# Kernel optimization log

Hardware: AMD Instinct MI355X
Metric: run time of the kernel (lower is better)

## Reference

```python
import jax, jax.numpy as jnp
import numpy as np

N, E, IN, H, D, ED = 50000, 800000, 128, 4, 16, 16
HD = H * D


def setup_inputs() -> dict:
    key = jax.random.key(0)
    ks = jax.random.split(key, 12)
    s_in = 1.0 / np.sqrt(IN).astype(np.float32)
    s_ed = 1.0 / np.sqrt(ED).astype(np.float32)
    return {
        "x": jax.random.normal(ks[0], (N, IN), jnp.float32),
        "edge_index": jax.random.randint(ks[1], (2, E), 0, N, dtype=jnp.int32),
        "edge_attr": jnp.ones((E, ED), jnp.float32),
        "Wq": jax.random.normal(ks[2], (IN, HD), jnp.float32) * s_in,
        "bq": jnp.zeros((HD,), jnp.float32),
        "Wk": jax.random.normal(ks[3], (IN, HD), jnp.float32) * s_in,
        "bk": jnp.zeros((HD,), jnp.float32),
        "Wv": jax.random.normal(ks[4], (IN, HD), jnp.float32) * s_in,
        "bv": jnp.zeros((HD,), jnp.float32),
        "We": jax.random.normal(ks[5], (ED, HD), jnp.float32) * s_ed,
        "Wskip": jax.random.normal(ks[6], (IN, HD), jnp.float32) * s_in,
        "bskip": jnp.zeros((HD,), jnp.float32),
    }


def reference(x, edge_index, edge_attr, Wq, bq, Wk, bk, Wv, bv, We, Wskip, bskip):
    n = x.shape[0]
    src, dst = edge_index[0], edge_index[1]  # x_j = src, x_i = dst (source_to_target)
    q = (x @ Wq + bq).reshape(n, H, D)
    k = (x @ Wk + bk).reshape(n, H, D)
    v = (x @ Wv + bv).reshape(n, H, D)
    e = (edge_attr @ We).reshape(-1, H, D)  # [E,H,D]

    k_j = k[src] + e                         # [E,H,D]
    v_j = v[src] + e                         # [E,H,D]
    q_i = q[dst]                             # [E,H,D]

    alpha = jnp.sum(q_i * k_j, axis=-1) / jnp.sqrt(jnp.float32(D))  # [E,H]
    # segment softmax over incoming edges per destination node
    amax = jax.ops.segment_max(alpha, dst, num_segments=n)          # [N,H]
    amax = jnp.where(jnp.isfinite(amax), amax, 0.0)
    ex = jnp.exp(alpha - amax[dst])                                 # [E,H]
    denom = jax.ops.segment_sum(ex, dst, num_segments=n)           # [N,H]
    alpha_sm = ex / (denom[dst] + 1e-16)                            # [E,H]

    msg = alpha_sm[..., None] * v_j                                 # [E,H,D]
    out = jax.ops.segment_sum(msg, dst, num_segments=n)            # [N,H,D]
    out = out.reshape(n, HD) + (x @ Wskip + bskip)                  # root/skip connection
    return out, edge_index, alpha_sm
```

## Files before the change

kernel.cpp:

```cpp
#include <hip/hip_runtime.h>


__global__ __launch_bounds__(256) void gemm_qkvs(
    const float* __restrict__ x,
    const float* __restrict__ Wq, const float* __restrict__ bq,
    const float* __restrict__ Wk, const float* __restrict__ bk,
    const float* __restrict__ Wv, const float* __restrict__ bv,
    const float* __restrict__ Wsk, const float* __restrict__ bsk,
    float* __restrict__ q, float* __restrict__ k, float* __restrict__ v,
    float* __restrict__ skip, float* __restrict__ macc,
    float* __restrict__ denom, int N)
{
    __shared__ float Xl[64 * 128];
    const int tid  = threadIdx.x;
    const int base = blockIdx.x * 64;
    const int nvalid = min(64, N - base);

    for (int i = tid; i < 64 * 32; i += 256) {
        int node = i >> 5;
        float4 val = make_float4(0.f, 0.f, 0.f, 0.f);
        if (node < nvalid)
            val = reinterpret_cast<const float4*>(x)[(size_t)(base + node) * 32 + (i & 31)];
        reinterpret_cast<float4*>(Xl)[i] = val;
    }
    __syncthreads();

    const int wave = tid >> 6;
    const int lane = tid & 63;
    const int c   = lane * 4;
    const int arr = c >> 6;
    const int cc  = c & 63;
    const float* W; const float* B; float* O;
    if (arr == 0)      { W = Wq;  B = bq;  O = q; }
    else if (arr == 1) { W = Wk;  B = bk;  O = k; }
    else if (arr == 2) { W = Wv;  B = bv;  O = v; }
    else               { W = Wsk; B = bsk; O = skip; }

    float acc[16][4];
    #pragma unroll
    for (int n = 0; n < 16; n++) {
        acc[n][0] = 0.f; acc[n][1] = 0.f; acc[n][2] = 0.f; acc[n][3] = 0.f;
    }

    const float* Xw = Xl + wave * 16 * 128;

    for (int kk = 0; kk < 128; kk += 4) {
        float4 w0 = *reinterpret_cast<const float4*>(W + (kk + 0) * 64 + cc);
        float4 w1 = *reinterpret_cast<const float4*>(W + (kk + 1) * 64 + cc);
        float4 w2 = *reinterpret_cast<const float4*>(W + (kk + 2) * 64 + cc);
        float4 w3 = *reinterpret_cast<const float4*>(W + (kk + 3) * 64 + cc);
        #pragma unroll
        for (int n = 0; n < 16; n++) {
            float4 xv = *reinterpret_cast<const float4*>(Xw + n * 128 + kk);
            acc[n][0] += xv.x * w0.x + xv.y * w1.x + xv.z * w2.x + xv.w * w3.x;
            acc[n][1] += xv.x * w0.y + xv.y * w1.y + xv.z * w2.y + xv.w * w3.y;
            acc[n][2] += xv.x * w0.z + xv.y * w1.z + xv.z * w2.z + xv.w * w3.z;
            acc[n][3] += xv.x * w0.w + xv.y * w1.w + xv.z * w2.w + xv.w * w3.w;
        }
    }

    const float4 zero4 = make_float4(0.f, 0.f, 0.f, 0.f);
    float4 bias = *reinterpret_cast<const float4*>(B + cc);
    #pragma unroll
    for (int n = 0; n < 16; n++) {
        int node = base + wave * 16 + n;
        if (node < N) {
            float4 r = make_float4(acc[n][0] + bias.x, acc[n][1] + bias.y,
                                   acc[n][2] + bias.z, acc[n][3] + bias.w);
            *reinterpret_cast<float4*>(O + (size_t)node * 64 + cc) = r;
            if (arr == 0)
                *reinterpret_cast<float4*>(macc + (size_t)node * 64 + cc) = zero4;
            if (arr == 1 && cc == 0)
                *reinterpret_cast<float4*>(denom + (size_t)node * 4) = zero4;
        }
    }
}

__global__ __launch_bounds__(256) void edge_fused(
    const int* __restrict__ ei, const float* __restrict__ ea,
    const float* __restrict__ We,
    const float* __restrict__ q, const float* __restrict__ k,
    const float* __restrict__ v,
    float* __restrict__ exa,
    float* __restrict__ denom,
    float* __restrict__ macc,
    int E)
{
    const int tid  = threadIdx.x;
    const int lane = tid & 63;

    float WeR[16];
    #pragma unroll
    for (int j = 0; j < 16; j++) WeR[j] = We[j * 64 + lane];

    const int ed = blockIdx.x * 4 + (tid >> 6);
    if (ed >= E) return;

    const int src = ei[ed];
    const int dst = ei[E + ed];

    const float4* eap = reinterpret_cast<const float4*>(ea + (size_t)ed * 16);
    float4 a0 = eap[0], a1 = eap[1], a2 = eap[2], a3 = eap[3];
    float et = a0.x * WeR[0]  + a0.y * WeR[1]  + a0.z * WeR[2]  + a0.w * WeR[3]
             + a1.x * WeR[4]  + a1.y * WeR[5]  + a1.z * WeR[6]  + a1.w * WeR[7]
             + a2.x * WeR[8]  + a2.y * WeR[9]  + a2.z * WeR[10] + a2.w * WeR[11]
             + a3.x * WeR[12] + a3.y * WeR[13] + a3.z * WeR[14] + a3.w * WeR[15];

    const float kj = k[(size_t)src * 64 + lane] + et;
    const float vj = v[(size_t)src * 64 + lane] + et;
    const float qi = q[(size_t)dst * 64 + lane];

    float p = qi * kj;
    p += __shfl_xor(p, 8);
    p += __shfl_xor(p, 4);
    p += __shfl_xor(p, 2);
    p += __shfl_xor(p, 1);

    const float e1 = __expf(p * 0.25f);

    atomicAdd(&macc[(size_t)dst * 64 + lane], e1 * vj);

    if ((lane & 15) == 0) {
        const int h = lane >> 4;
        exa[(size_t)ed * 4 + h] = e1;
        atomicAdd(&denom[(size_t)dst * 4 + h], e1);
    }
}

__global__ __launch_bounds__(256) void fin_edges(
    const int* __restrict__ ei, const float* __restrict__ denom,
    float* __restrict__ asm_io, float* __restrict__ ei_out, int E)
{
    int e = blockIdx.x * 256 + threadIdx.x;
    if (e >= E) return;
    int s = ei[e];
    int d = ei[E + e];

    float4 a  = *reinterpret_cast<float4*>(asm_io + (size_t)e * 4);
    float4 dn = *reinterpret_cast<const float4*>(denom + (size_t)d * 4);
    a.x /= (dn.x + 1e-16f);
    a.y /= (dn.y + 1e-16f);
    a.z /= (dn.z + 1e-16f);
    a.w /= (dn.w + 1e-16f);
    *reinterpret_cast<float4*>(asm_io + (size_t)e * 4) = a;

    ei_out[e]     = (float)s;
    ei_out[E + e] = (float)d;
}

__global__ __launch_bounds__(256) void fin_out(
    const float* __restrict__ skip, const float* __restrict__ denom,
    float* __restrict__ out_io, int total)
{
    int i = blockIdx.x * 256 + threadIdx.x;
    if (i >= total) return;
    int node = i >> 6, h = (i & 63) >> 4;
    out_io[i] = out_io[i] / (denom[node * 4 + h] + 1e-16f) + skip[i];
}

extern "C" void kernel_launch(void* const* d_in, const int* in_sizes, int n_in,
                              void* d_out, int out_size, void* d_ws, size_t ws_size,
                              hipStream_t stream)
{
    const float* x   = (const float*)d_in[0];
    const int*   ei  = (const int*)  d_in[1];
    const float* ea  = (const float*)d_in[2];
    const float* Wq  = (const float*)d_in[3];
    const float* bq  = (const float*)d_in[4];
    const float* Wk  = (const float*)d_in[5];
    const float* bk  = (const float*)d_in[6];
    const float* Wv  = (const float*)d_in[7];
    const float* bv  = (const float*)d_in[8];
    const float* We  = (const float*)d_in[9];
    const float* Wsk = (const float*)d_in[10];
    const float* bsk = (const float*)d_in[11];

    const int N = in_sizes[0] / 128;
    const int E = in_sizes[1] / 2;

    float* out     = (float*)d_out;
    float* ei_out  = out + (size_t)N * 64;
    float* asm_out = ei_out + (size_t)2 * E;

    float* q     = (float*)d_ws;
    float* k     = q + (size_t)N * 64;
    float* v     = k + (size_t)N * 64;
    float* skip  = v + (size_t)N * 64;
    float* denom = skip + (size_t)N * 64;

    int nb1 = (N + 63) / 64;
    gemm_qkvs<<<nb1, 256, 0, stream>>>(x, Wq, bq, Wk, bk, Wv, bv, Wsk, bsk,
                                       q, k, v, skip, out, denom, N);

    int nb2 = (E + 3) / 4;
    edge_fused<<<nb2, 256, 0, stream>>>(ei, ea, We, q, k, v, asm_out, denom, out, E);

    fin_edges<<<(E + 255) / 256, 256, 0, stream>>>(ei, denom, asm_out, ei_out, E);
    fin_out<<<(N * 64 + 255) / 256, 256, 0, stream>>>(skip, denom, out, N * 64);
}
```

Before: 502.5 us.

## Store q/k/v in fp16 and process two edges per wave

The projection kernel now writes q, k and v as half precision, which halves the bytes moved by the random gathers in the edge kernel. The skip projection stays fp32. The GEMM tile shrinks from 64 to 32 nodes per block, and each wave in the edge kernel now handles two edges, so more independent loads and atomics are in flight. The cost is fp16 rounding error on the attention logits and messages, plus more register use per edge thread.

```diff
diff --git a/kernel.cpp b/kernel.cpp
--- a/kernel.cpp
+++ b/kernel.cpp
@@ -1,5 +1,7 @@
 #include <hip/hip_runtime.h>
 
+
+typedef __attribute__((ext_vector_type(4))) _Float16 half4;
 
 __global__ __launch_bounds__(256) void gemm_qkvs(
     const float* __restrict__ x,
@@ -7,16 +9,17 @@
     const float* __restrict__ Wk, const float* __restrict__ bk,
     const float* __restrict__ Wv, const float* __restrict__ bv,
     const float* __restrict__ Wsk, const float* __restrict__ bsk,
-    float* __restrict__ q, float* __restrict__ k, float* __restrict__ v,
+    _Float16* __restrict__ qh, _Float16* __restrict__ kh,
+    _Float16* __restrict__ vh,
     float* __restrict__ skip, float* __restrict__ macc,
     float* __restrict__ denom, int N)
 {
-    __shared__ float Xl[64 * 128];
+    __shared__ float Xl[32 * 128];
     const int tid  = threadIdx.x;
-    const int base = blockIdx.x * 64;
-    const int nvalid = min(64, N - base);
-
-    for (int i = tid; i < 64 * 32; i += 256) {
+    const int base = blockIdx.x * 32;
+    const int nvalid = min(32, N - base);
+
+    for (int i = tid; i < 32 * 32; i += 256) {
         int node = i >> 5;
         float4 val = make_float4(0.f, 0.f, 0.f, 0.f);
         if (node < nvalid)
@@ -30,19 +33,19 @@
     const int c   = lane * 4;
     const int arr = c >> 6;
     const int cc  = c & 63;
-    const float* W; const float* B; float* O;
-    if (arr == 0)      { W = Wq;  B = bq;  O = q; }
-    else if (arr == 1) { W = Wk;  B = bk;  O = k; }
-    else if (arr == 2) { W = Wv;  B = bv;  O = v; }
-    else               { W = Wsk; B = bsk; O = skip; }
-
-    float acc[16][4];
+    const float* W; const float* B;
+    if (arr == 0)      { W = Wq;  B = bq;  }
+    else if (arr == 1) { W = Wk;  B = bk;  }
+    else if (arr == 2) { W = Wv;  B = bv;  }
+    else               { W = Wsk; B = bsk; }
+
+    float acc[8][4];
     #pragma unroll
-    for (int n = 0; n < 16; n++) {
+    for (int n = 0; n < 8; n++) {
         acc[n][0] = 0.f; acc[n][1] = 0.f; acc[n][2] = 0.f; acc[n][3] = 0.f;
     }
 
-    const float* Xw = Xl + wave * 16 * 128;
+    const float* Xw = Xl + wave * 8 * 128;
 
     for (int kk = 0; kk < 128; kk += 4) {
         float4 w0 = *reinterpret_cast<const float4*>(W + (kk + 0) * 64 + cc);
@@ -50,7 +53,7 @@
         float4 w2 = *reinterpret_cast<const float4*>(W + (kk + 2) * 64 + cc);
         float4 w3 = *reinterpret_cast<const float4*>(W + (kk + 3) * 64 + cc);
         #pragma unroll
-        for (int n = 0; n < 16; n++) {
+        for (int n = 0; n < 8; n++) {
             float4 xv = *reinterpret_cast<const float4*>(Xw + n * 128 + kk);
             acc[n][0] += xv.x * w0.x + xv.y * w1.x + xv.z * w2.x + xv.w * w3.x;
             acc[n][1] += xv.x * w0.y + xv.y * w1.y + xv.z * w2.y + xv.w * w3.y;
@@ -62,16 +65,29 @@
     const float4 zero4 = make_float4(0.f, 0.f, 0.f, 0.f);
     float4 bias = *reinterpret_cast<const float4*>(B + cc);
     #pragma unroll
-    for (int n = 0; n < 16; n++) {
-        int node = base + wave * 16 + n;
+    for (int n = 0; n < 8; n++) {
+        int node = base + wave * 8 + n;
         if (node < N) {
             float4 r = make_float4(acc[n][0] + bias.x, acc[n][1] + bias.y,
                                    acc[n][2] + bias.z, acc[n][3] + bias.w);
-            *reinterpret_cast<float4*>(O + (size_t)node * 64 + cc) = r;
-            if (arr == 0)
-                *reinterpret_cast<float4*>(macc + (size_t)node * 64 + cc) = zero4;
-            if (arr == 1 && cc == 0)
-                *reinterpret_cast<float4*>(denom + (size_t)node * 4) = zero4;
+            size_t off = (size_t)node * 64 + cc;
+            if (arr == 3) {
+                *reinterpret_cast<float4*>(skip + off) = r;
+            } else {
+                half4 hv;
+                hv.x = (_Float16)r.x; hv.y = (_Float16)r.y;
+                hv.z = (_Float16)r.z; hv.w = (_Float16)r.w;
+                if (arr == 0) {
+                    *reinterpret_cast<half4*>(qh + off) = hv;
+                    *reinterpret_cast<float4*>(macc + off) = zero4;
+                } else if (arr == 1) {
+                    *reinterpret_cast<half4*>(kh + off) = hv;
+                    if (cc == 0)
+                        *reinterpret_cast<float4*>(denom + (size_t)node * 4) = zero4;
+                } else {
+                    *reinterpret_cast<half4*>(vh + off) = hv;
+                }
+            }
         }
     }
 }
@@ -79,8 +95,8 @@
 __global__ __launch_bounds__(256) void edge_fused(
     const int* __restrict__ ei, const float* __restrict__ ea,
     const float* __restrict__ We,
-    const float* __restrict__ q, const float* __restrict__ k,
-    const float* __restrict__ v,
+    const _Float16* __restrict__ qh, const _Float16* __restrict__ kh,
+    const _Float16* __restrict__ vh,
     float* __restrict__ exa,
     float* __restrict__ denom,
     float* __restrict__ macc,
@@ -93,37 +109,63 @@
     #pragma unroll
     for (int j = 0; j < 16; j++) WeR[j] = We[j * 64 + lane];
 
-    const int ed = blockIdx.x * 4 + (tid >> 6);
-    if (ed >= E) return;
-
-    const int src = ei[ed];
-    const int dst = ei[E + ed];
-
-    const float4* eap = reinterpret_cast<const float4*>(ea + (size_t)ed * 16);
-    float4 a0 = eap[0], a1 = eap[1], a2 = eap[2], a3 = eap[3];
-    float et = a0.x * WeR[0]  + a0.y * WeR[1]  + a0.z * WeR[2]  + a0.w * WeR[3]
-             + a1.x * WeR[4]  + a1.y * WeR[5]  + a1.z * WeR[6]  + a1.w * WeR[7]
-             + a2.x * WeR[8]  + a2.y * WeR[9]  + a2.z * WeR[10] + a2.w * WeR[11]
-             + a3.x * WeR[12] + a3.y * WeR[13] + a3.z * WeR[14] + a3.w * WeR[15];
-
-    const float kj = k[(size_t)src * 64 + lane] + et;
-    const float vj = v[(size_t)src * 64 + lane] + et;
-    const float qi = q[(size_t)dst * 64 + lane];
-
-    float p = qi * kj;
-    p += __shfl_xor(p, 8);
-    p += __shfl_xor(p, 4);
-    p += __shfl_xor(p, 2);
-    p += __shfl_xor(p, 1);
-
-    const float e1 = __expf(p * 0.25f);
-
-    atomicAdd(&macc[(size_t)dst * 64 + lane], e1 * vj);
-
+    const int ed0 = (blockIdx.x * 4 + (tid >> 6)) * 2;
+    if (ed0 >= E) return;
+    const bool two = (ed0 + 1) < E;
+    const int ed1 = two ? ed0 + 1 : ed0;
+
+    const int src0 = ei[ed0], dst0 = ei[E + ed0];
+    const int src1 = ei[ed1], dst1 = ei[E + ed1];
+
+    const float k0 = (float)kh[(size_t)src0 * 64 + lane];
+    const float v0 = (float)vh[(size_t)src0 * 64 + lane];
+    const float q0 = (float)qh[(size_t)dst0 * 64 + lane];
+    const float k1 = (float)kh[(size_t)src1 * 64 + lane];
+    const float v1 = (float)vh[(size_t)src1 * 64 + lane];
+    const float q1 = (float)qh[(size_t)dst1 * 64 + lane];
+
+    const float4* ea0 = reinterpret_cast<const float4*>(ea + (size_t)ed0 * 16);
+    const float4* ea1 = reinterpret_cast<const float4*>(ea + (size_t)ed1 * 16);
+    float4 a0 = ea0[0], a1 = ea0[1], a2 = ea0[2], a3 = ea0[3];
+    float4 b0 = ea1[0], b1 = ea1[1], b2 = ea1[2], b3 = ea1[3];
+
+    float et0 = a0.x * WeR[0]  + a0.y * WeR[1]  + a0.z * WeR[2]  + a0.w * WeR[3]
+              + a1.x * WeR[4]  + a1.y * WeR[5]  + a1.z * WeR[6]  + a1.w * WeR[7]
+              + a2.x * WeR[8]  + a2.y * WeR[9]  + a2.z * WeR[10] + a2.w * WeR[11]
+              + a3.x * WeR[12] + a3.y * WeR[13] + a3.z * WeR[14] + a3.w * WeR[15];
+    float et1 = b0.x * WeR[0]  + b0.y * WeR[1]  + b0.z * WeR[2]  + b0.w * WeR[3]
+              + b1.x * WeR[4]  + b1.y * WeR[5]  + b1.z * WeR[6]  + b1.w * WeR[7]
+              + b2.x * WeR[8]  + b2.y * WeR[9]  + b2.z * WeR[10] + b2.w * WeR[11]
+              + b3.x * WeR[12] + b3.y * WeR[13] + b3.z * WeR[14] + b3.w * WeR[15];
+
+    float p0 = q0 * (k0 + et0);
+    p0 += __shfl_xor(p0, 8);
+    p0 += __shfl_xor(p0, 4);
+    p0 += __shfl_xor(p0, 2);
+    p0 += __shfl_xor(p0, 1);
+    const float e10 = __expf(p0 * 0.25f);
+
+    float p1 = q1 * (k1 + et1);
+    p1 += __shfl_xor(p1, 8);
+    p1 += __shfl_xor(p1, 4);
+    p1 += __shfl_xor(p1, 2);
+    p1 += __shfl_xor(p1, 1);
+    const float e11 = __expf(p1 * 0.25f);
+
+    atomicAdd(&macc[(size_t)dst0 * 64 + lane], e10 * (v0 + et0));
     if ((lane & 15) == 0) {
         const int h = lane >> 4;
-        exa[(size_t)ed * 4 + h] = e1;
-        atomicAdd(&denom[(size_t)dst * 4 + h], e1);
+        exa[(size_t)ed0 * 4 + h] = e10;
+        atomicAdd(&denom[(size_t)dst0 * 4 + h], e10);
+    }
+
+    if (two) {
+        atomicAdd(&macc[(size_t)dst1 * 64 + lane], e11 * (v1 + et1));
+        if ((lane & 15) == 0) {
+            const int h = lane >> 4;
+            exa[(size_t)ed1 * 4 + h] = e11;
+            atomicAdd(&denom[(size_t)dst1 * 4 + h], e11);
+        }
     }
 }
 
@@ -182,18 +224,19 @@
     float* ei_out  = out + (size_t)N * 64;
     float* asm_out = ei_out + (size_t)2 * E;
 
-    float* q     = (float*)d_ws;
-    float* k     = q + (size_t)N * 64;
-    float* v     = k + (size_t)N * 64;
-    float* skip  = v + (size_t)N * 64;
-    float* denom = skip + (size_t)N * 64;
-
-    int nb1 = (N + 63) / 64;
+    float*    skip  = (float*)d_ws;
+    float*    denom = skip + (size_t)N * 64;
+    _Float16* qh    = (_Float16*)(denom + (size_t)N * 4);
+    _Float16* kh    = qh + (size_t)N * 64;
+    _Float16* vh    = kh + (size_t)N * 64;
+
+    int nb1 = (N + 31) / 32;
     gemm_qkvs<<<nb1, 256, 0, stream>>>(x, Wq, bq, Wk, bk, Wv, bv, Wsk, bsk,
-                                       q, k, v, skip, out, denom, N);
-
-    int nb2 = (E + 3) / 4;
-    edge_fused<<<nb2, 256, 0, stream>>>(ei, ea, We, q, k, v, asm_out, denom, out, E);
+                                       qh, kh, vh, skip, out, denom, N);
+
+    int nb2 = (E + 7) / 8;
+    edge_fused<<<nb2, 256, 0, stream>>>(ei, ea, We, qh, kh, vh,
+                                        asm_out, denom, out, E);
 
     fin_edges<<<(E + 255) / 256, 256, 0, stream>>>(ei, denom, asm_out, ei_out, E);
     fin_out<<<(N * 64 + 255) / 256, 256, 0, stream>>>(skip, denom, out, N * 64);
```

Result: faster. 431.3 us (-14.2%).
